# Performance work log

Measured on AMD Instinct MI355X. Metric: run time of the kernel, lower is better.

## Reference

```python
import jax, jax.numpy as jnp
import numpy as np

PAD_token, SOS_token, EOS_token = 0, 1, 2
V, E, H, B, To, Ti = 10000, 512, 512, 32, 256, 1024


def _u(key, shape, fan_in):
    s = 1.0 / np.sqrt(fan_in)
    return jax.random.uniform(key, shape, jnp.float32, -s, s)


def setup_inputs() -> dict:
    key = jax.random.key(0)
    ks = jax.random.split(key, 16)
    inp = {
        "padded_input": jax.random.randint(ks[0], (B, To), 3, V),
        "encoder_padded_outputs": jax.random.normal(ks[1], (B, Ti, H), jnp.float32),
        "embedding": jax.random.normal(ks[2], (V, E), jnp.float32) * 0.02,
        # layer 0 LSTMCell: input = embed + encoder context (E + H)
        "Wih0": _u(ks[3], (4 * H, E + H), H), "Whh0": _u(ks[4], (4 * H, H), H),
        "bih0": _u(ks[5], (4 * H,), H),       "bhh0": _u(ks[6], (4 * H,), H),
        # layer 1 LSTMCell: input = H
        "Wih1": _u(ks[7], (4 * H, H), H),     "Whh1": _u(ks[8], (4 * H, H), H),
        "bih1": _u(ks[9], (4 * H,), H),       "bhh1": _u(ks[10], (4 * H,), H),
        # MLP: Linear(2H -> H), Tanh, Linear(H -> V)
        "W1": _u(ks[11], (H, 2 * H), 2 * H),  "b1": _u(ks[12], (H,), 2 * H),
        "W2": _u(ks[13], (V, H), H),          "b2": _u(ks[14], (V,), H),
    }
    return inp


def _lstm_cell(x, h, c, Wih, Whh, bih, bhh):
    g = x @ Wih.T + bih + h @ Whh.T + bhh            # [B, 4H]
    i, f, gg, o = jnp.split(g, 4, axis=-1)           # torch gate order i,f,g,o
    c2 = jax.nn.sigmoid(f) * c + jax.nn.sigmoid(i) * jnp.tanh(gg)
    h2 = jax.nn.sigmoid(o) * jnp.tanh(c2)
    return h2, c2


def reference(padded_input, encoder_padded_outputs, embedding,
              Wih0, Whh0, bih0, bhh0, Wih1, Whh1, bih1, bhh1,
              W1, b1, W2, b2):
    n = padded_input.shape[0]
    sos = jnp.full((n, 1), SOS_token, padded_input.dtype)
    eos = jnp.full((n, 1), EOS_token, padded_input.dtype)
    ys_in = jnp.concatenate([sos, padded_input], axis=1)   # [B, To+1]
    ys_out = jnp.concatenate([padded_input, eos], axis=1)  # [B, To+1]

    emb = embedding[ys_in]                                 # [B, To+1, E]
    emb_t = jnp.swapaxes(emb, 0, 1)                        # [To+1, B, E]
    enc = encoder_padded_outputs                           # [B, Ti, H]

    h0 = jnp.zeros((n, H), enc.dtype)
    init = (h0, h0, h0, h0, jnp.zeros((n, enc.shape[2]), enc.dtype))

    def step(carry, e_t):
        h_0, c_0, h_1, c_1, att_c = carry
        rnn_in = jnp.concatenate([e_t, att_c], axis=1)
        h_0, c_0 = _lstm_cell(rnn_in, h_0, c_0, Wih0, Whh0, bih0, bhh0)
        h_1, c_1 = _lstm_cell(h_0, h_1, c_1, Wih1, Whh1, bih1, bhh1)
        scores = jnp.einsum('bh,bth->bt', h_1, enc)        # [B, Ti]
        att_w = jax.nn.softmax(scores, axis=-1)
        att_c = jnp.einsum('bt,bth->bh', att_w, enc)       # [B, H]
        mlp_in = jnp.concatenate([h_1, att_c], axis=1)
        logits = jnp.tanh(mlp_in @ W1.T + b1) @ W2.T + b2  # [B, V]
        return (h_0, c_0, h_1, c_1, att_c), logits

    _, y_all = jax.lax.scan(step, init, emb_t)             # [To+1, B, V]
    logits = jnp.swapaxes(y_all, 0, 1).reshape(-1, V)      # [B*(To+1), V]
    labels = ys_out.reshape(-1)
    logp = jax.nn.log_softmax(logits, axis=-1)
    nll = -jnp.take_along_axis(logp, labels[:, None], axis=1)[:, 0]
    mask = (labels != PAD_token).astype(logits.dtype)
    loss = jnp.sum(nll * mask) / jnp.maximum(jnp.sum(mask), 1.0)
    return loss
```

## Files before the change

### kernel.cpp

```cpp
#include <hip/hip_runtime.h>
#include <hip/hip_bf16.h>

#define B_    32
#define TO_   256
#define T_    257
#define H_    512
#define V_    10000
#define TI_   1024
#define NROW_ 8224
#define NB_   256

using f32x4 = __attribute__((ext_vector_type(4))) float;
using s16x8 = __attribute__((ext_vector_type(8))) short;

struct Ptrs {
  const int* padded;
  const float* enc;
  const float* emb;
  const float *Wih0, *Whh0, *bih0, *bhh0;
  const float *Wih1, *Whh1, *bih1, *bhh1;
  const float *W1, *b1, *W2, *b2;
  float* out;
  unsigned short *mlpin;
  unsigned short *embt;
  unsigned short *tanhv;
  unsigned short *W0c;
  unsigned short *W1c;
  unsigned short *W1b;
  unsigned short *W2b;
  float *bias0c, *bias1c;
  float *u;
  unsigned short *Xh0;
  unsigned short *Xh1;
  float *Xh1f;
  float *Zb;
  unsigned *bar;
  float *rowsum;
  float *lablog;
};

__device__ __forceinline__ unsigned short f2b(float f){
  __hip_bfloat16 h = __float2bfloat16(f);
  unsigned short r; __builtin_memcpy(&r, &h, 2); return r;
}
__device__ __forceinline__ float b2f(unsigned short u){
  unsigned v = ((unsigned)u) << 16; float f; __builtin_memcpy(&f, &v, 4); return f;
}
__device__ __forceinline__ float sigf(float x){ return 1.f / (1.f + expf(-x)); }

__device__ __forceinline__ float aldf(const float* p){
  return __hip_atomic_load(p, __ATOMIC_RELAXED, __HIP_MEMORY_SCOPE_AGENT);
}
__device__ __forceinline__ unsigned aldw(const unsigned* p){
  return __hip_atomic_load(p, __ATOMIC_RELAXED, __HIP_MEMORY_SCOPE_AGENT);
}
__device__ __forceinline__ unsigned long long aldu(const unsigned long long* p){
  return __hip_atomic_load(p, __ATOMIC_RELAXED, __HIP_MEMORY_SCOPE_AGENT);
}
__device__ __forceinline__ void astf(float* p, float v){
  __hip_atomic_store(p, v, __ATOMIC_RELAXED, __HIP_MEMORY_SCOPE_AGENT);
}
__device__ __forceinline__ void astu(unsigned long long* p, unsigned long long v){
  __hip_atomic_store(p, v, __ATOMIC_RELAXED, __HIP_MEMORY_SCOPE_AGENT);
}
__device__ __forceinline__ void astw(unsigned* p, unsigned v){
  __hip_atomic_store(p, v, __ATOMIC_RELAXED, __HIP_MEMORY_SCOPE_AGENT);
}

__device__ __forceinline__ void gbar(unsigned* bar, unsigned ph){
  asm volatile("s_waitcnt vmcnt(0)" ::: "memory");
  __syncthreads();
  if (threadIdx.x < 64){
    const int l = threadIdx.x;
    if (l == 0) astw(bar + blockIdx.x * 4, ph);
    for (;;){
      unsigned f0 = aldw(bar + (l      ) * 4);
      unsigned f1 = aldw(bar + (l +  64) * 4);
      unsigned f2 = aldw(bar + (l + 128) * 4);
      unsigned f3 = aldw(bar + (l + 192) * 4);
      bool ok = (f0 >= ph) & (f1 >= ph) & (f2 >= ph) & (f3 >= ph);
      if (__all(ok)) break;
      __builtin_amdgcn_s_sleep(2);
    }
  }
  __syncthreads();
}

__device__ __forceinline__ void gbar128(unsigned* bar, unsigned ph){
  asm volatile("s_waitcnt vmcnt(0)" ::: "memory");
  __syncthreads();
  if (threadIdx.x < 64){
    const int l = threadIdx.x;
    if (l == 0) astw(bar + blockIdx.x * 4, ph);
    for (;;){
      unsigned f0 = aldw(bar + (l     ) * 4);
      unsigned f1 = aldw(bar + (l + 64) * 4);
      bool ok = (f0 >= ph) & (f1 >= ph);
      if (__all(ok)) break;
      __builtin_amdgcn_s_sleep(2);
    }
  }
  __syncthreads();
}

__global__ __launch_bounds__(256) void kprep(Ptrs P){
  const int stride = gridDim.x * blockDim.x;
  const int i0 = blockIdx.x * blockDim.x + threadIdx.x;
  for (int i = i0; i < 2048; i += stride) P.bar[i] = 0u;
  for (int i = i0; i < T_ * B_ * 512; i += stride){
    int k = i & 511, tb = i >> 9, b = tb & 31, t = tb >> 5;
    int tok = (t == 0) ? 1 : P.padded[b * TO_ + (t - 1)];
    P.embt[i] = f2b(P.emb[(size_t)tok * 512 + k]);
  }
  for (int i = i0; i < 2048 * 1536; i += stride){
    int k = i % 1536, gp = i / 1536;
    int j = gp >> 2, q = gp & 3, g = q * 512 + j;
    float v = (k < 1024) ? P.Wih0[(size_t)g * 1024 + k] : P.Whh0[(size_t)g * 512 + (k - 1024)];
    P.W0c[i] = f2b(v);
  }
  for (int i = i0; i < 2048 * 1024; i += stride){
    int k = i & 1023, gp = i >> 10;
    int j = gp >> 2, q = gp & 3, g = q * 512 + j;
    float v = (k < 512) ? P.Wih1[(size_t)g * 512 + k] : P.Whh1[(size_t)g * 512 + (k - 512)];
    P.W1c[i] = f2b(v);
  }
  for (int i = i0; i < 2048; i += stride){
    int j = i >> 2, q = i & 3, g = q * 512 + j;
    P.bias0c[i] = P.bih0[g] + P.bhh0[g];
    P.bias1c[i] = P.bih1[g] + P.bhh1[g];
  }
  for (int i = i0; i < 512 * 1024; i += stride) P.W1b[i] = f2b(P.W1[i]);
  for (int i = i0; i < NROW_; i += stride) P.rowsum[i] = 0.f;
}

__global__ __launch_bounds__(256) void kprep2(Ptrs P){
  const int stride = gridDim.x * blockDim.x;
  const int i0 = blockIdx.x * blockDim.x + threadIdx.x;
  for (int i = i0; i < V_ * 512; i += stride) P.W2b[i] = f2b(P.W2[i]);
}

__global__ __launch_bounds__(256, 1) void kA(Ptrs P){
  __shared__ __align__(16) unsigned short enc_s[128 * 512];
  __shared__ float h1_s[512];
  __shared__ float w_s[128];
  __shared__ float gate_s[32][17];
  __shared__ float h_s[32][4];
  const int bb = blockIdx.x, tid = threadIdx.x;
  const int b_att = bb >> 3;

  {
    const float* ep = P.enc + ((size_t)b_att * TI_ + (size_t)(bb & 7) * 128) * H_;
    for (int idx = tid; idx < 128 * 512; idx += 256){
      int r = idx >> 9;
      unsigned byteoff = ((unsigned)idx * 2u) ^ ((unsigned)(r & 7) << 4);
      enc_s[byteoff >> 1] = f2b(ep[idx]);
    }
  }
  {
    int g = bb * 256 + tid;
    if (g < 32768){ astf(P.u + g, 0.f); astf(P.Xh1f + g, 0.f); }
    if (g < 16384){ astw((unsigned*)P.Xh0 + g, 0u); astw((unsigned*)P.Xh1 + g, 0u); }
    if (g < 64) astf(P.Zb + g, (g >= 32) ? 1.f : 0.f);
  }
  gbar(P.bar, 1u);

  const int wv = tid >> 6;
  const int l  = tid & 63, lr = l & 15, lk = l >> 4;
  const int eidx = tid - 128;
  const int eb = eidx >> 2, ejl = eidx & 3;
  float c0r = 0.f, c1r = 0.f;

  for (int t = 0; t < T_; ++t){
    const int p = t & 1, pp = p ^ 1;
    const unsigned phb = 3u * (unsigned)t;
    if (bb < 128){
      if (wv < 2){
        const int batch = wv * 16 + lr;
        const unsigned short* Brow = P.W0c + (size_t)(bb * 16 + lr) * 1536;
        const unsigned short* Erow = P.embt + ((size_t)t * 32 + batch) * 512;
        const float* Urow = P.u + pp * 16384 + batch * 512;
        const unsigned long long* Hrow =
            (const unsigned long long*)(P.Xh0 + pp * 16384 + batch * 512);
        const float rZ = 1.f / aldf(P.Zb + pp * 32 + batch);
        f32x4 acc = {0.f, 0.f, 0.f, 0.f};
        #pragma unroll
        for (int ks = 0; ks < 16; ++ks){
          s16x8 a = *(const s16x8*)(Erow + ks * 32 + lk * 8);
          s16x8 b = *(const s16x8*)(Brow + ks * 32 + lk * 8);
          acc = __builtin_amdgcn_mfma_f32_16x16x32_bf16(a, b, acc, 0, 0, 0);
        }
        #pragma unroll
        for (int ks = 0; ks < 16; ++ks){
          const int kb = ks * 32 + lk * 8;
          unsigned long long dd[4];
          dd[0] = aldu((const unsigned long long*)(Urow + kb));
          dd[1] = aldu((const unsigned long long*)(Urow + kb + 2));
          dd[2] = aldu((const unsigned long long*)(Urow + kb + 4));
          dd[3] = aldu((const unsigned long long*)(Urow + kb + 6));
          float uf[8]; __builtin_memcpy(uf, dd, 32);
          s16x8 a;
          #pragma unroll
          for (int e = 0; e < 8; ++e) a[e] = (short)f2b(uf[e] * rZ);
          s16x8 b = *(const s16x8*)(Brow + 512 + kb);
          acc = __builtin_amdgcn_mfma_f32_16x16x32_bf16(a, b, acc, 0, 0, 0);
        }
        #pragma unroll
        for (int ks = 0; ks < 16; ++ks){
          const int kb = ks * 32 + lk * 8;
          unsigned long long dd[2];
          dd[0] = aldu(Hrow + (kb >> 2));
          dd[1] = aldu(Hrow + (kb >> 2) + 1);
          s16x8 a; __builtin_memcpy(&a, dd, 16);
          s16x8 b = *(const s16x8*)(Brow + 1024 + kb);
          acc = __builtin_amdgcn_mfma_f32_16x16x32_bf16(a, b, acc, 0, 0, 0);
        }
        #pragma unroll
        for (int j = 0; j < 4; ++j) gate_s[wv * 16 + lk * 4 + j][lr] = acc[j];
      }
    } else if (bb < 160){
      if (t > 0){
        const int b = bb - 128;
        const float rZ = 1.f / aldf(P.Zb + pp * 32 + b);
        unsigned long long v = aldu((const unsigned long long*)(P.u + pp * 16384 + b * 512) + tid);
        float f2[2]; __builtin_memcpy(f2, &v, 8);
        unsigned pk = (unsigned)f2b(f2[0] * rZ) | ((unsigned)f2b(f2[1] * rZ) << 16);
        *(unsigned*)(P.mlpin + ((size_t)(t - 1) * 32 + b) * 1024 + 512 + tid * 2) = pk;
      }
    } else if (bb < 224){
      astf(P.u + p * 16384 + (bb - 160) * 256 + tid, 0.f);
    } else if (bb == 224 && tid < 32){
      astf(P.Zb + p * 32 + tid, 0.f);
    }
    if (bb < 128){
      __syncthreads();
      if (tid >= 128){
        const float* bs = P.bias0c + bb * 16 + ejl * 4;
        float ii = sigf (gate_s[eb][ejl * 4 + 0] + bs[0]);
        float ff = sigf (gate_s[eb][ejl * 4 + 1] + bs[1]);
        float gg = tanhf(gate_s[eb][ejl * 4 + 2] + bs[2]);
        float oo = sigf (gate_s[eb][ejl * 4 + 3] + bs[3]);
        float cn = ff * c0r + ii * gg; c0r = cn;
        h_s[eb][ejl] = oo * tanhf(cn);
      }
      __syncthreads();
      if (tid < 32){
        unsigned short hb[4];
        #pragma unroll
        for (int jl = 0; jl < 4; ++jl) hb[jl] = f2b(h_s[tid][jl]);
        unsigned long long v; __builtin_memcpy(&v, hb, 8);
        astu((unsigned long long*)(P.Xh0 + p * 16384 + tid * 512 + bb * 4), v);
      }
      gbar128(P.bar, phb + 2u);
    }
    if (bb < 128){
      if (wv < 2){
        const int batch = wv * 16 + lr;
        const unsigned short* Brow = P.W1c + (size_t)(bb * 16 + lr) * 1024;
        const unsigned long long* H0r =
            (const unsigned long long*)(P.Xh0 + p * 16384 + batch * 512);
        const unsigned long long* H1r =
            (const unsigned long long*)(P.Xh1 + pp * 16384 + batch * 512);
        f32x4 acc = {0.f, 0.f, 0.f, 0.f};
        #pragma unroll
        for (int ks = 0; ks < 16; ++ks){
          const int kb = ks * 32 + lk * 8;
          unsigned long long dd[2];
          dd[0] = aldu(H0r + (kb >> 2));
          dd[1] = aldu(H0r + (kb >> 2) + 1);
          s16x8 a; __builtin_memcpy(&a, dd, 16);
          s16x8 b = *(const s16x8*)(Brow + kb);
          acc = __builtin_amdgcn_mfma_f32_16x16x32_bf16(a, b, acc, 0, 0, 0);
        }
        #pragma unroll
        for (int ks = 0; ks < 16; ++ks){
          const int kb = ks * 32 + lk * 8;
          unsigned long long dd[2];
          dd[0] = aldu(H1r + (kb >> 2));
          dd[1] = aldu(H1r + (kb >> 2) + 1);
          s16x8 a; __builtin_memcpy(&a, dd, 16);
          s16x8 b = *(const s16x8*)(Brow + 512 + kb);
          acc = __builtin_amdgcn_mfma_f32_16x16x32_bf16(a, b, acc, 0, 0, 0);
        }
        #pragma unroll
        for (int j = 0; j < 4; ++j) gate_s[wv * 16 + lk * 4 + j][lr] = acc[j];
      }
      __syncthreads();
      if (tid >= 128){
        const float* bs = P.bias1c + bb * 16 + ejl * 4;
        float ii = sigf (gate_s[eb][ejl * 4 + 0] + bs[0]);
        float ff = sigf (gate_s[eb][ejl * 4 + 1] + bs[1]);
        float gg = tanhf(gate_s[eb][ejl * 4 + 2] + bs[2]);
        float oo = sigf (gate_s[eb][ejl * 4 + 3] + bs[3]);
        float cn = ff * c1r + ii * gg; c1r = cn;
        h_s[eb][ejl] = oo * tanhf(cn);
      }
      __syncthreads();
      if (tid < 32){
        unsigned short hb[4];
        #pragma unroll
        for (int jl = 0; jl < 4; ++jl) hb[jl] = f2b(h_s[tid][jl]);
        unsigned long long vb; __builtin_memcpy(&vb, hb, 8);
        astu((unsigned long long*)(P.Xh1 + p * 16384 + tid * 512 + bb * 4), vb);
        *(unsigned long long*)(P.mlpin + ((size_t)t * 32 + tid) * 1024 + bb * 4) = vb;
        unsigned long long w0, w1;
        __builtin_memcpy(&w0, &h_s[tid][0], 8);
        __builtin_memcpy(&w1, &h_s[tid][2], 8);
        unsigned long long* dst = (unsigned long long*)P.Xh1f + ((p * 16384 + tid * 512 + bb * 4) >> 1);
        astu(dst, w0); astu(dst + 1, w1);
      }
    }
    gbar(P.bar, phb + 3u);
    {
      unsigned long long v = aldu((const unsigned long long*)(P.Xh1f + p * 16384 + b_att * 512) + tid);
      float f2[2]; __builtin_memcpy(f2, &v, 8);
      h1_s[tid * 2] = f2[0]; h1_s[tid * 2 + 1] = f2[1];
    }
    __syncthreads();
    {
      const int ti_l = tid >> 1, half = tid & 1;
      float s = 0.f;
      const unsigned swz = (unsigned)(ti_l & 7) << 4;
      for (int h8 = half * 256; h8 < half * 256 + 256; h8 += 8){
        unsigned byteoff = ((unsigned)(ti_l * 512 + h8) * 2u) ^ swz;
        s16x8 ev = *(const s16x8*)((const char*)enc_s + byteoff);
        #pragma unroll
        for (int e = 0; e < 8; ++e) s += b2f((unsigned short)ev[e]) * h1_s[h8 + e];
      }
      s += __shfl_xor(s, 1);
      if (half == 0) w_s[ti_l] = expf(s);
    }
    __syncthreads();
    {
      if (tid < 128){
        float z = w_s[tid];
        #pragma unroll
        for (int off = 1; off < 64; off <<= 1) z += __shfl_xor(z, off);
        if ((tid & 63) == 0) unsafeAtomicAdd(P.Zb + p * 32 + b_att, z);
      }
      float a0 = 0.f, a1 = 0.f;
      const int hc = tid * 2;
      for (int ti = 0; ti < 128; ++ti){
        const float wvv = w_s[ti];
        unsigned byteoff = ((unsigned)(ti * 1024 + hc * 2)) ^ ((unsigned)(ti & 7) << 4);
        unsigned pk = *(const unsigned*)((const char*)enc_s + byteoff);
        a0 += wvv * b2f((unsigned short)(pk & 0xffffu));
        a1 += wvv * b2f((unsigned short)(pk >> 16));
      }
      unsafeAtomicAdd(P.u + p * 16384 + b_att * 512 + hc, a0);
      unsafeAtomicAdd(P.u + p * 16384 + b_att * 512 + hc + 1, a1);
    }
    gbar(P.bar, phb + 4u);
  }
  if (bb >= 128 && bb < 160){
    const int b = bb - 128;
    const float rZ = 1.f / aldf(P.Zb + 0 * 32 + b);
    unsigned long long v = aldu((const unsigned long long*)(P.u + 0 * 16384 + b * 512) + tid);
    float f2[2]; __builtin_memcpy(f2, &v, 8);
    unsigned pk = (unsigned)f2b(f2[0] * rZ) | ((unsigned)f2b(f2[1] * rZ) << 16);
    *(unsigned*)(P.mlpin + ((size_t)256 * 32 + b) * 1024 + 512 + tid * 2) = pk;
  }
}

__global__ __launch_bounds__(256) void kB1(Ptrs P){
  const int wid = blockIdx.x * 4 + (threadIdx.x >> 6);
  if (wid >= 129 * 8) return;
  const int mt = wid >> 3, nt = wid & 7;
  const int l = threadIdx.x & 63, lr = l & 15, lk = l >> 4;
  const int mr = mt * 64, nc = nt * 64;
  f32x4 acc[4][4] = {};
  for (int k0 = 0; k0 < 1024; k0 += 32){
    s16x8 af[4], bfm[4];
    #pragma unroll
    for (int f = 0; f < 4; ++f){
      int row = mr + f * 16 + lr; if (row > NROW_ - 1) row = NROW_ - 1;
      af[f] = *(const s16x8*)(P.mlpin + (size_t)row * 1024 + k0 + lk * 8);
      int col = nc + f * 16 + lr;
      bfm[f] = *(const s16x8*)(P.W1b + (size_t)col * 1024 + k0 + lk * 8);
    }
    #pragma unroll
    for (int fi = 0; fi < 4; ++fi)
      #pragma unroll
      for (int fj = 0; fj < 4; ++fj)
        acc[fi][fj] = __builtin_amdgcn_mfma_f32_16x16x32_bf16(af[fi], bfm[fj], acc[fi][fj], 0, 0, 0);
  }
  #pragma unroll
  for (int fi = 0; fi < 4; ++fi){
    #pragma unroll
    for (int jj = 0; jj < 4; ++jj){
      int m = mr + fi * 16 + lk * 4 + jj;
      if (m >= NROW_) continue;
      #pragma unroll
      for (int fj = 0; fj < 4; ++fj){
        int n = nc + fj * 16 + lr;
        P.tanhv[(size_t)m * 512 + n] = f2b(tanhf(acc[fi][fj][jj] + P.b1[n]));
      }
    }
  }
}

__global__ __launch_bounds__(256) void kB2(Ptrs P){
  const int wid = blockIdx.x * 4 + (threadIdx.x >> 6);
  if (wid >= 129 * 157) return;
  const int mt = wid / 157, nt = wid % 157;
  const int l = threadIdx.x & 63, lr = l & 15, lk = l >> 4;
  const int mr = mt * 64, nc = nt * 64;
  f32x4 acc[4][4] = {};
  for (int k0 = 0; k0 < 512; k0 += 32){
    s16x8 af[4], bfm[4];
    #pragma unroll
    for (int f = 0; f < 4; ++f){
      int row = mr + f * 16 + lr; if (row > NROW_ - 1) row = NROW_ - 1;
      af[f] = *(const s16x8*)(P.tanhv + (size_t)row * 512 + k0 + lk * 8);
      int col = nc + f * 16 + lr; if (col > V_ - 1) col = V_ - 1;
      bfm[f] = *(const s16x8*)(P.W2b + (size_t)col * 512 + k0 + lk * 8);
    }
    #pragma unroll
    for (int fi = 0; fi < 4; ++fi)
      #pragma unroll
      for (int fj = 0; fj < 4; ++fj)
        acc[fi][fj] = __builtin_amdgcn_mfma_f32_16x16x32_bf16(af[fi], bfm[fj], acc[fi][fj], 0, 0, 0);
  }
  #pragma unroll
  for (int fi = 0; fi < 4; ++fi){
    #pragma unroll
    for (int jj = 0; jj < 4; ++jj){
      const int m = mr + fi * 16 + lk * 4 + jj;
      float s = 0.f;
      #pragma unroll
      for (int fj = 0; fj < 4; ++fj){
        int n = nc + fj * 16 + lr;
        if (n < V_) s += expf(acc[fi][fj][jj] + P.b2[n]);
      }
      s += __shfl_xor(s, 1); s += __shfl_xor(s, 2);
      s += __shfl_xor(s, 4); s += __shfl_xor(s, 8);
      if (lr == 0 && m < NROW_) unsafeAtomicAdd(P.rowsum + m, s);
    }
  }
}

__global__ __launch_bounds__(256) void kL1(Ptrs P){
  const int wid = blockIdx.x * 4 + (threadIdx.x >> 6);
  if (wid >= NROW_) return;
  const int l = threadIdx.x & 63;
  const int t = wid >> 5, b = wid & 31;
  const int lab = (t < TO_) ? P.padded[b * TO_ + t] : 2;
  float s = 0.f;
  s16x8 av = *(const s16x8*)(P.tanhv + (size_t)wid * 512 + l * 8);
  s16x8 wv = *(const s16x8*)(P.W2b + (size_t)lab * 512 + l * 8);
  #pragma unroll
  for (int e = 0; e < 8; ++e) s += b2f((unsigned short)av[e]) * b2f((unsigned short)wv[e]);
  #pragma unroll
  for (int off = 1; off < 64; off <<= 1) s += __shfl_xor(s, off);
  if (l == 0) P.lablog[wid] = s + P.b2[lab];
}

__global__ __launch_bounds__(512) void kL2(Ptrs P){
  __shared__ float ssum[8], scnt[8];
  const int tid = threadIdx.x;
  float sum = 0.f, cnt = 0.f;
  for (int r = tid; r < NROW_; r += 512){
    int t = r >> 5, b = r & 31;
    int lab = (t < TO_) ? P.padded[b * TO_ + t] : 2;
    if (lab != 0){ sum += logf(P.rowsum[r]) - P.lablog[r]; cnt += 1.f; }
  }
  #pragma unroll
  for (int off = 1; off < 64; off <<= 1){ sum += __shfl_xor(sum, off); cnt += __shfl_xor(cnt, off); }
  if ((tid & 63) == 0){ ssum[tid >> 6] = sum; scnt[tid >> 6] = cnt; }
  __syncthreads();
  if (tid == 0){
    float S = 0.f, C = 0.f;
    for (int i = 0; i < 8; ++i){ S += ssum[i]; C += scnt[i]; }
    P.out[0] = S / fmaxf(C, 1.f);
  }
}

extern "C" void kernel_launch(void* const* d_in, const int* in_sizes, int n_in,
                              void* d_out, int out_size, void* d_ws, size_t ws_size,
                              hipStream_t stream){
  (void)in_sizes; (void)n_in; (void)out_size; (void)ws_size;
  Ptrs P;
  P.padded = (const int*)d_in[0];
  P.enc    = (const float*)d_in[1];
  P.emb    = (const float*)d_in[2];
  P.Wih0 = (const float*)d_in[3];  P.Whh0 = (const float*)d_in[4];
  P.bih0 = (const float*)d_in[5];  P.bhh0 = (const float*)d_in[6];
  P.Wih1 = (const float*)d_in[7];  P.Whh1 = (const float*)d_in[8];
  P.bih1 = (const float*)d_in[9];  P.bhh1 = (const float*)d_in[10];
  P.W1 = (const float*)d_in[11];   P.b1 = (const float*)d_in[12];
  P.W2 = (const float*)d_in[13];   P.b2 = (const float*)d_in[14];
  P.out = (float*)d_out;

  char* w = (char*)d_ws;
  size_t off = 0;
  auto take = [&](size_t bytes) -> void* {
    void* ptr = (void*)(w + off);
    off += (bytes + 255) & ~(size_t)255;
    return ptr;
  };
  P.mlpin  = (unsigned short*)take((size_t)T_ * B_ * 1024 * 2);
  P.embt   = (unsigned short*)take((size_t)T_ * B_ * 512 * 2);
  P.tanhv  = P.embt;
  P.W0c    = (unsigned short*)take((size_t)2048 * 1536 * 2);
  P.W1c    = (unsigned short*)take((size_t)2048 * 1024 * 2);
  P.W2b    = P.W0c;
  P.W1b    = (unsigned short*)take((size_t)512 * 1024 * 2);
  P.bias0c = (float*)take(2048 * 4);
  P.bias1c = (float*)take(2048 * 4);
  P.u      = (float*)take(2 * 32 * 512 * 4);
  P.Xh0    = (unsigned short*)take(2 * 32 * 512 * 2);
  P.Xh1    = (unsigned short*)take(2 * 32 * 512 * 2);
  P.Xh1f   = (float*)take(2 * 32 * 512 * 4);
  P.Zb     = (float*)take(2 * 32 * 4);
  P.bar    = (unsigned*)take(8192);
  P.rowsum = (float*)take(NROW_ * 4);
  P.lablog = (float*)take(NROW_ * 4);

  kprep<<<dim3(2048), dim3(256), 0, stream>>>(P);
  void* args[] = { (void*)&P };
  hipLaunchCooperativeKernel(kA, dim3(NB_), dim3(256), args, 0, stream);
  kprep2<<<dim3(1024), dim3(256), 0, stream>>>(P);
  kB1<<<dim3(258),  dim3(256), 0, stream>>>(P);
  kB2<<<dim3(5064), dim3(256), 0, stream>>>(P);
  kL1<<<dim3(2056), dim3(256), 0, stream>>>(P);
  kL2<<<dim3(1),    dim3(512), 0, stream>>>(P);
}
```

Baseline: 9.451 ms.

## Replace global barriers with targeted flag sync and deterministic attention reduction

Replaces the three full-grid barriers per timestep in the persistent recurrent kernel with point-to-point arrival flags. Layer-0 GEMM blocks wait only on the 32 reducer blocks, the two LSTM layers sync among the 128 GEMM blocks, and attention blocks wait on layer-1 completion. Attention partial sums and softmax denominators are written to per-chunk slots and summed by 32 reducer blocks, replacing global float atomics and the zeroing passes they required. The LSTM GEMMs are also split across all four waves along K, with results combined in shared memory. This aims to cut barrier latency on the sequential critical path, at the cost of more complex dependency reasoning and a risk of ordering bugs.

```diff
diff --git a/kernel.cpp b/kernel.cpp
--- a/kernel.cpp
+++ b/kernel.cpp
@@ -12,6 +12,7 @@
 
 using f32x4 = __attribute__((ext_vector_type(4))) float;
 using s16x8 = __attribute__((ext_vector_type(8))) short;
+typedef unsigned long long ull;
 
 struct Ptrs {
   const int* padded;
@@ -29,12 +30,17 @@
   unsigned short *W1b;
   unsigned short *W2b;
   float *bias0c, *bias1c;
-  float *u;
+  unsigned short *attc;
+  float *upart;
+  float *zp;
   unsigned short *Xh0;
   unsigned short *Xh1;
   float *Xh1f;
-  float *Zb;
-  unsigned *bar;
+  unsigned *arrX;
+  unsigned *arrY;
+  unsigned *marr;
+  unsigned *larr;
+  unsigned *ibar;
   float *rowsum;
   float *lablog;
 };
@@ -54,50 +60,32 @@
 __device__ __forceinline__ unsigned aldw(const unsigned* p){
   return __hip_atomic_load(p, __ATOMIC_RELAXED, __HIP_MEMORY_SCOPE_AGENT);
 }
-__device__ __forceinline__ unsigned long long aldu(const unsigned long long* p){
+__device__ __forceinline__ ull aldu(const ull* p){
   return __hip_atomic_load(p, __ATOMIC_RELAXED, __HIP_MEMORY_SCOPE_AGENT);
 }
 __device__ __forceinline__ void astf(float* p, float v){
   __hip_atomic_store(p, v, __ATOMIC_RELAXED, __HIP_MEMORY_SCOPE_AGENT);
 }
-__device__ __forceinline__ void astu(unsigned long long* p, unsigned long long v){
+__device__ __forceinline__ void astu(ull* p, ull v){
   __hip_atomic_store(p, v, __ATOMIC_RELAXED, __HIP_MEMORY_SCOPE_AGENT);
 }
 __device__ __forceinline__ void astw(unsigned* p, unsigned v){
   __hip_atomic_store(p, v, __ATOMIC_RELAXED, __HIP_MEMORY_SCOPE_AGENT);
 }
-
-__device__ __forceinline__ void gbar(unsigned* bar, unsigned ph){
-  asm volatile("s_waitcnt vmcnt(0)" ::: "memory");
-  __syncthreads();
+#define DRAIN asm volatile("s_waitcnt vmcnt(0)" ::: "memory")
+
+__device__ __forceinline__ void gbarInit(unsigned* bar){
+  DRAIN; __syncthreads();
   if (threadIdx.x < 64){
     const int l = threadIdx.x;
-    if (l == 0) astw(bar + blockIdx.x * 4, ph);
+    if (l == 0) astw(bar + blockIdx.x * 4, 1u);
     for (;;){
       unsigned f0 = aldw(bar + (l      ) * 4);
       unsigned f1 = aldw(bar + (l +  64) * 4);
       unsigned f2 = aldw(bar + (l + 128) * 4);
       unsigned f3 = aldw(bar + (l + 192) * 4);
-      bool ok = (f0 >= ph) & (f1 >= ph) & (f2 >= ph) & (f3 >= ph);
-      if (__all(ok)) break;
-      __builtin_amdgcn_s_sleep(2);
-    }
-  }
-  __syncthreads();
-}
-
-__device__ __forceinline__ void gbar128(unsigned* bar, unsigned ph){
-  asm volatile("s_waitcnt vmcnt(0)" ::: "memory");
-  __syncthreads();
-  if (threadIdx.x < 64){
-    const int l = threadIdx.x;
-    if (l == 0) astw(bar + blockIdx.x * 4, ph);
-    for (;;){
-      unsigned f0 = aldw(bar + (l     ) * 4);
-      unsigned f1 = aldw(bar + (l + 64) * 4);
-      bool ok = (f0 >= ph) & (f1 >= ph);
-      if (__all(ok)) break;
-      __builtin_amdgcn_s_sleep(2);
+      if (__all((f0 >= 1u) & (f1 >= 1u) & (f2 >= 1u) & (f3 >= 1u))) break;
+      __builtin_amdgcn_s_sleep(1);
     }
   }
   __syncthreads();
@@ -106,7 +94,9 @@
 __global__ __launch_bounds__(256) void kprep(Ptrs P){
   const int stride = gridDim.x * blockDim.x;
   const int i0 = blockIdx.x * blockDim.x + threadIdx.x;
-  for (int i = i0; i < 2048; i += stride) P.bar[i] = 0u;
+  for (int i = i0; i < 128 * 4; i += stride){ P.arrX[i] = 0u; P.arrY[i] = 0u; }
+  for (int i = i0; i < 256 * 4; i += stride){ P.marr[i] = 0u; P.ibar[i] = 0u; }
+  for (int i = i0; i < 32 * 4; i += stride) P.larr[i] = 0u;
   for (int i = i0; i < T_ * B_ * 512; i += stride){
     int k = i & 511, tb = i >> 9, b = tb & 31, t = tb >> 5;
     int tok = (t == 0) ? 1 : P.padded[b * TO_ + (t - 1)];
@@ -143,13 +133,14 @@
   __shared__ __align__(16) unsigned short enc_s[128 * 512];
   __shared__ float h1_s[512];
   __shared__ float w_s[128];
-  __shared__ float gate_s[32][17];
+  __shared__ float gate_s[2][32][17];
   __shared__ float h_s[32][4];
+  __shared__ float zred[2];
   const int bb = blockIdx.x, tid = threadIdx.x;
-  const int b_att = bb >> 3;
+  const int b_att = bb >> 3, tc = bb & 7;
 
   {
-    const float* ep = P.enc + ((size_t)b_att * TI_ + (size_t)(bb & 7) * 128) * H_;
+    const float* ep = P.enc + ((size_t)b_att * TI_ + (size_t)tc * 128) * H_;
     for (int idx = tid; idx < 128 * 512; idx += 256){
       int r = idx >> 9;
       unsigned byteoff = ((unsigned)idx * 2u) ^ ((unsigned)(r & 7) << 4);
@@ -158,87 +149,72 @@
   }
   {
     int g = bb * 256 + tid;
-    if (g < 32768){ astf(P.u + g, 0.f); astf(P.Xh1f + g, 0.f); }
     if (g < 16384){ astw((unsigned*)P.Xh0 + g, 0u); astw((unsigned*)P.Xh1 + g, 0u); }
-    if (g < 64) astf(P.Zb + g, (g >= 32) ? 1.f : 0.f);
-  }
-  gbar(P.bar, 1u);
-
-  const int wv = tid >> 6;
-  const int l  = tid & 63, lr = l & 15, lk = l >> 4;
-  const int eidx = tid - 128;
-  const int eb = eidx >> 2, ejl = eidx & 3;
+    if (g < 32768) astf(P.Xh1f + g, 0.f);
+    if (g < 8192)  astw((unsigned*)P.attc + g, 0u);
+  }
+  gbarInit(P.ibar);
+
+  const int wv = tid >> 6, l = tid & 63, lr = l & 15, lk = l >> 4;
+  const int bh = wv & 1, kh = wv >> 1;
+  const int batch = bh * 16 + lr;
+  const int eidx = tid - 128, eb = eidx >> 2, ejl = eidx & 3;
+  const bool isGemm = bb < 128;
+  const int rb = bb - 128; const bool isRed = (rb >= 0 && rb < 32);
   float c0r = 0.f, c1r = 0.f;
 
   for (int t = 0; t < T_; ++t){
     const int p = t & 1, pp = p ^ 1;
-    const unsigned phb = 3u * (unsigned)t;
-    if (bb < 128){
-      if (wv < 2){
-        const int batch = wv * 16 + lr;
+    const unsigned tv = (unsigned)t + 1u;
+    if (isGemm){
+      if (t > 0 && tid < 64){
+        const unsigned want = tv - 1u;
+        for (;;){
+          unsigned f = (tid < 32) ? aldw(P.larr + tid * 4) : want;
+          if (__all(f >= want)) break;
+          __builtin_amdgcn_s_sleep(1);
+        }
+      }
+      __syncthreads();
+      {
         const unsigned short* Brow = P.W0c + (size_t)(bb * 16 + lr) * 1536;
         const unsigned short* Erow = P.embt + ((size_t)t * 32 + batch) * 512;
-        const float* Urow = P.u + pp * 16384 + batch * 512;
-        const unsigned long long* Hrow =
-            (const unsigned long long*)(P.Xh0 + pp * 16384 + batch * 512);
-        const float rZ = 1.f / aldf(P.Zb + pp * 32 + batch);
+        const ull* Arow = (const ull*)(P.attc + batch * 512);
+        const ull* Hrow = (const ull*)(P.Xh0 + pp * 16384 + batch * 512);
         f32x4 acc = {0.f, 0.f, 0.f, 0.f};
         #pragma unroll
-        for (int ks = 0; ks < 16; ++ks){
-          s16x8 a = *(const s16x8*)(Erow + ks * 32 + lk * 8);
-          s16x8 b = *(const s16x8*)(Brow + ks * 32 + lk * 8);
+        for (int ks = 0; ks < 8; ++ks){
+          const int kb = (kh * 8 + ks) * 32 + lk * 8;
+          s16x8 a = *(const s16x8*)(Erow + kb);
+          s16x8 b = *(const s16x8*)(Brow + kb);
           acc = __builtin_amdgcn_mfma_f32_16x16x32_bf16(a, b, acc, 0, 0, 0);
         }
         #pragma unroll
-        for (int ks = 0; ks < 16; ++ks){
-          const int kb = ks * 32 + lk * 8;
-          unsigned long long dd[4];
-          dd[0] = aldu((const unsigned long long*)(Urow + kb));
-          dd[1] = aldu((const unsigned long long*)(Urow + kb + 2));
-          dd[2] = aldu((const unsigned long long*)(Urow + kb + 4));
-          dd[3] = aldu((const unsigned long long*)(Urow + kb + 6));
-          float uf[8]; __builtin_memcpy(uf, dd, 32);
-          s16x8 a;
-          #pragma unroll
-          for (int e = 0; e < 8; ++e) a[e] = (short)f2b(uf[e] * rZ);
+        for (int ks = 0; ks < 8; ++ks){
+          const int kb = (kh * 8 + ks) * 32 + lk * 8;
+          ull d0 = aldu(Arow + (kb >> 2)), d1 = aldu(Arow + (kb >> 2) + 1);
+          s16x8 a; __builtin_memcpy(&a, &d0, 8); __builtin_memcpy(((char*)&a) + 8, &d1, 8);
           s16x8 b = *(const s16x8*)(Brow + 512 + kb);
           acc = __builtin_amdgcn_mfma_f32_16x16x32_bf16(a, b, acc, 0, 0, 0);
         }
         #pragma unroll
-        for (int ks = 0; ks < 16; ++ks){
-          const int kb = ks * 32 + lk * 8;
-          unsigned long long dd[2];
-          dd[0] = aldu(Hrow + (kb >> 2));
-          dd[1] = aldu(Hrow + (kb >> 2) + 1);
-          s16x8 a; __builtin_memcpy(&a, dd, 16);
+        for (int ks = 0; ks < 8; ++ks){
+          const int kb = (kh * 8 + ks) * 32 + lk * 8;
+          ull d0 = aldu(Hrow + (kb >> 2)), d1 = aldu(Hrow + (kb >> 2) + 1);
+          s16x8 a; __builtin_memcpy(&a, &d0, 8); __builtin_memcpy(((char*)&a) + 8, &d1, 8);
           s16x8 b = *(const s16x8*)(Brow + 1024 + kb);
           acc = __builtin_amdgcn_mfma_f32_16x16x32_bf16(a, b, acc, 0, 0, 0);
         }
         #pragma unroll
-        for (int j = 0; j < 4; ++j) gate_s[wv * 16 + lk * 4 + j][lr] = acc[j];
-      }
-    } else if (bb < 160){
-      if (t > 0){
-        const int b = bb - 128;
-        const float rZ = 1.f / aldf(P.Zb + pp * 32 + b);
-        unsigned long long v = aldu((const unsigned long long*)(P.u + pp * 16384 + b * 512) + tid);
-        float f2[2]; __builtin_memcpy(f2, &v, 8);
-        unsigned pk = (unsigned)f2b(f2[0] * rZ) | ((unsigned)f2b(f2[1] * rZ) << 16);
-        *(unsigned*)(P.mlpin + ((size_t)(t - 1) * 32 + b) * 1024 + 512 + tid * 2) = pk;
-      }
-    } else if (bb < 224){
-      astf(P.u + p * 16384 + (bb - 160) * 256 + tid, 0.f);
-    } else if (bb == 224 && tid < 32){
-      astf(P.Zb + p * 32 + tid, 0.f);
-    }
-    if (bb < 128){
+        for (int j = 0; j < 4; ++j) gate_s[kh][bh * 16 + lk * 4 + j][lr] = acc[j];
+      }
       __syncthreads();
       if (tid >= 128){
         const float* bs = P.bias0c + bb * 16 + ejl * 4;
-        float ii = sigf (gate_s[eb][ejl * 4 + 0] + bs[0]);
-        float ff = sigf (gate_s[eb][ejl * 4 + 1] + bs[1]);
-        float gg = tanhf(gate_s[eb][ejl * 4 + 2] + bs[2]);
-        float oo = sigf (gate_s[eb][ejl * 4 + 3] + bs[3]);
+        float ii = sigf (gate_s[0][eb][ejl * 4 + 0] + gate_s[1][eb][ejl * 4 + 0] + bs[0]);
+        float ff = sigf (gate_s[0][eb][ejl * 4 + 1] + gate_s[1][eb][ejl * 4 + 1] + bs[1]);
+        float gg = tanhf(gate_s[0][eb][ejl * 4 + 2] + gate_s[1][eb][ejl * 4 + 2] + bs[2]);
+        float oo = sigf (gate_s[0][eb][ejl * 4 + 3] + gate_s[1][eb][ejl * 4 + 3] + bs[3]);
         float cn = ff * c0r + ii * gg; c0r = cn;
         h_s[eb][ejl] = oo * tanhf(cn);
       }
@@ -247,50 +223,50 @@
         unsigned short hb[4];
         #pragma unroll
         for (int jl = 0; jl < 4; ++jl) hb[jl] = f2b(h_s[tid][jl]);
-        unsigned long long v; __builtin_memcpy(&v, hb, 8);
-        astu((unsigned long long*)(P.Xh0 + p * 16384 + tid * 512 + bb * 4), v);
-      }
-      gbar128(P.bar, phb + 2u);
-    }
-    if (bb < 128){
-      if (wv < 2){
-        const int batch = wv * 16 + lr;
+        ull v; __builtin_memcpy(&v, hb, 8);
+        astu((ull*)(P.Xh0 + p * 16384 + tid * 512 + bb * 4), v);
+      }
+      DRAIN; __syncthreads();
+      if (tid < 64){
+        if (tid == 0) astw(P.arrX + bb * 4, tv);
+        for (;;){
+          unsigned f0 = aldw(P.arrX + tid * 4), f1 = aldw(P.arrX + (tid + 64) * 4);
+          if (__all((f0 >= tv) & (f1 >= tv))) break;
+          __builtin_amdgcn_s_sleep(1);
+        }
+      }
+      __syncthreads();
+      {
         const unsigned short* Brow = P.W1c + (size_t)(bb * 16 + lr) * 1024;
-        const unsigned long long* H0r =
-            (const unsigned long long*)(P.Xh0 + p * 16384 + batch * 512);
-        const unsigned long long* H1r =
-            (const unsigned long long*)(P.Xh1 + pp * 16384 + batch * 512);
+        const ull* H0r = (const ull*)(P.Xh0 + p * 16384 + batch * 512);
+        const ull* H1r = (const ull*)(P.Xh1 + pp * 16384 + batch * 512);
         f32x4 acc = {0.f, 0.f, 0.f, 0.f};
         #pragma unroll
-        for (int ks = 0; ks < 16; ++ks){
-          const int kb = ks * 32 + lk * 8;
-          unsigned long long dd[2];
-          dd[0] = aldu(H0r + (kb >> 2));
-          dd[1] = aldu(H0r + (kb >> 2) + 1);
-          s16x8 a; __builtin_memcpy(&a, dd, 16);
+        for (int ks = 0; ks < 8; ++ks){
+          const int kb = (kh * 8 + ks) * 32 + lk * 8;
+          ull d0 = aldu(H0r + (kb >> 2)), d1 = aldu(H0r + (kb >> 2) + 1);
+          s16x8 a; __builtin_memcpy(&a, &d0, 8); __builtin_memcpy(((char*)&a) + 8, &d1, 8);
           s16x8 b = *(const s16x8*)(Brow + kb);
           acc = __builtin_amdgcn_mfma_f32_16x16x32_bf16(a, b, acc, 0, 0, 0);
         }
         #pragma unroll
-        for (int ks = 0; ks < 16; ++ks){
-          const int kb = ks * 32 + lk * 8;
-          unsigned long long dd[2];
-          dd[0] = aldu(H1r + (kb >> 2));
-          dd[1] = aldu(H1r + (kb >> 2) + 1);
-          s16x8 a; __builtin_memcpy(&a, dd, 16);
+        for (int ks = 0; ks < 8; ++ks){
+          const int kb = (kh * 8 + ks) * 32 + lk * 8;
+          ull d0 = aldu(H1r + (kb >> 2)), d1 = aldu(H1r + (kb >> 2) + 1);
+          s16x8 a; __builtin_memcpy(&a, &d0, 8); __builtin_memcpy(((char*)&a) + 8, &d1, 8);
           s16x8 b = *(const s16x8*)(Brow + 512 + kb);
           acc = __builtin_amdgcn_mfma_f32_16x16x32_bf16(a, b, acc, 0, 0, 0);
         }
         #pragma unroll
-        for (int j = 0; j < 4; ++j) gate_s[wv * 16 + lk * 4 + j][lr] = acc[j];
+        for (int j = 0; j < 4; ++j) gate_s[kh][bh * 16 + lk * 4 + j][lr] = acc[j];
       }
       __syncthreads();
       if (tid >= 128){
         const float* bs = P.bias1c + bb * 16 + ejl * 4;
-        float ii = sigf (gate_s[eb][ejl * 4 + 0] + bs[0]);
-        float ff = sigf (gate_s[eb][ejl * 4 + 1] + bs[1]);
-        float gg = tanhf(gate_s[eb][ejl * 4 + 2] + bs[2]);
-        float oo = sigf (gate_s[eb][ejl * 4 + 3] + bs[3]);
+        float ii = sigf (gate_s[0][eb][ejl * 4 + 0] + gate_s[1][eb][ejl * 4 + 0] + bs[0]);
+        float ff = sigf (gate_s[0][eb][ejl * 4 + 1] + gate_s[1][eb][ejl * 4 + 1] + bs[1]);
+        float gg = tanhf(gate_s[0][eb][ejl * 4 + 2] + gate_s[1][eb][ejl * 4 + 2] + bs[2]);
+        float oo = sigf (gate_s[0][eb][ejl * 4 + 3] + gate_s[1][eb][ejl * 4 + 3] + bs[3]);
         float cn = ff * c1r + ii * gg; c1r = cn;
         h_s[eb][ejl] = oo * tanhf(cn);
       }
@@ -299,19 +275,28 @@
         unsigned short hb[4];
         #pragma unroll
         for (int jl = 0; jl < 4; ++jl) hb[jl] = f2b(h_s[tid][jl]);
-        unsigned long long vb; __builtin_memcpy(&vb, hb, 8);
-        astu((unsigned long long*)(P.Xh1 + p * 16384 + tid * 512 + bb * 4), vb);
-        *(unsigned long long*)(P.mlpin + ((size_t)t * 32 + tid) * 1024 + bb * 4) = vb;
-        unsigned long long w0, w1;
+        ull vb; __builtin_memcpy(&vb, hb, 8);
+        astu((ull*)(P.Xh1 + p * 16384 + tid * 512 + bb * 4), vb);
+        *(ull*)(P.mlpin + ((size_t)t * 32 + tid) * 1024 + bb * 4) = vb;
+        ull w0, w1;
         __builtin_memcpy(&w0, &h_s[tid][0], 8);
         __builtin_memcpy(&w1, &h_s[tid][2], 8);
-        unsigned long long* dst = (unsigned long long*)P.Xh1f + ((p * 16384 + tid * 512 + bb * 4) >> 1);
+        ull* dst = (ull*)P.Xh1f + ((p * 16384 + tid * 512 + bb * 4) >> 1);
         astu(dst, w0); astu(dst + 1, w1);
       }
-    }
-    gbar(P.bar, phb + 3u);
+      DRAIN; __syncthreads();
+      if (tid == 0) astw(P.arrY + bb * 4, tv);
+    }
+    if (tid < 64){
+      for (;;){
+        unsigned f0 = aldw(P.arrY + tid * 4), f1 = aldw(P.arrY + (tid + 64) * 4);
+        if (__all((f0 >= tv) & (f1 >= tv))) break;
+        __builtin_amdgcn_s_sleep(1);
+      }
+    }
+    __syncthreads();
     {
-      unsigned long long v = aldu((const unsigned long long*)(P.Xh1f + p * 16384 + b_att * 512) + tid);
+      ull v = aldu((const ull*)(P.Xh1f + p * 16384 + b_att * 512) + tid);
       float f2[2]; __builtin_memcpy(f2, &v, 8);
       h1_s[tid * 2] = f2[0]; h1_s[tid * 2 + 1] = f2[1];
     }
@@ -335,7 +320,7 @@
         float z = w_s[tid];
         #pragma unroll
         for (int off = 1; off < 64; off <<= 1) z += __shfl_xor(z, off);
-        if ((tid & 63) == 0) unsafeAtomicAdd(P.Zb + p * 32 + b_att, z);
+        if ((tid & 63) == 0) zred[tid >> 6] = z;
       }
       float a0 = 0.f, a1 = 0.f;
       const int hc = tid * 2;
@@ -346,18 +331,39 @@
         a0 += wvv * b2f((unsigned short)(pk & 0xffffu));
         a1 += wvv * b2f((unsigned short)(pk >> 16));
       }
-      unsafeAtomicAdd(P.u + p * 16384 + b_att * 512 + hc, a0);
-      unsafeAtomicAdd(P.u + p * 16384 + b_att * 512 + hc + 1, a1);
-    }
-    gbar(P.bar, phb + 4u);
-  }
-  if (bb >= 128 && bb < 160){
-    const int b = bb - 128;
-    const float rZ = 1.f / aldf(P.Zb + 0 * 32 + b);
-    unsigned long long v = aldu((const unsigned long long*)(P.u + 0 * 16384 + b * 512) + tid);
-    float f2[2]; __builtin_memcpy(f2, &v, 8);
-    unsigned pk = (unsigned)f2b(f2[0] * rZ) | ((unsigned)f2b(f2[1] * rZ) << 16);
-    *(unsigned*)(P.mlpin + ((size_t)256 * 32 + b) * 1024 + 512 + tid * 2) = pk;
+      float f2[2] = {a0, a1};
+      ull pv; __builtin_memcpy(&pv, f2, 8);
+      astu((ull*)(P.upart + ((size_t)b_att * 8 + tc) * 512 + hc), pv);
+      __syncthreads();
+      if (tid == 0) astf(P.zp + b_att * 8 + tc, zred[0] + zred[1]);
+      DRAIN; __syncthreads();
+      if (tid == 0) astw(P.marr + (b_att * 8 + tc) * 4, tv);
+    }
+    if (isRed){
+      if (tid < 64){
+        for (;;){
+          unsigned f = (tid < 8) ? aldw(P.marr + (rb * 8 + tid) * 4) : tv;
+          if (__all(f >= tv)) break;
+          __builtin_amdgcn_s_sleep(1);
+        }
+      }
+      __syncthreads();
+      const int hc = tid * 2;
+      float s0 = 0.f, s1 = 0.f, zs = 0.f;
+      #pragma unroll
+      for (int c = 0; c < 8; ++c){
+        ull v = aldu((const ull*)(P.upart + ((size_t)rb * 8 + c) * 512 + hc));
+        float f2[2]; __builtin_memcpy(f2, &v, 8);
+        s0 += f2[0]; s1 += f2[1];
+        zs += aldf(P.zp + rb * 8 + c);
+      }
+      const float rZ = 1.f / zs;
+      unsigned pk = (unsigned)f2b(s0 * rZ) | ((unsigned)f2b(s1 * rZ) << 16);
+      astw(((unsigned*)P.attc) + rb * 256 + tid, pk);
+      *(unsigned*)(P.mlpin + ((size_t)t * 32 + rb) * 1024 + 512 + hc) = pk;
+      DRAIN; __syncthreads();
+      if (tid == 0) astw(P.larr + rb * 4, tv);
+    }
   }
 }
 
@@ -506,12 +512,17 @@
   P.W1b    = (unsigned short*)take((size_t)512 * 1024 * 2);
   P.bias0c = (float*)take(2048 * 4);
   P.bias1c = (float*)take(2048 * 4);
-  P.u      = (float*)take(2 * 32 * 512 * 4);
+  P.attc   = (unsigned short*)take(32 * 512 * 2);
+  P.upart  = (float*)take((size_t)32 * 8 * 512 * 4);
+  P.zp     = (float*)take(32 * 8 * 4);
   P.Xh0    = (unsigned short*)take(2 * 32 * 512 * 2);
   P.Xh1    = (unsigned short*)take(2 * 32 * 512 * 2);
   P.Xh1f   = (float*)take(2 * 32 * 512 * 4);
-  P.Zb     = (float*)take(2 * 32 * 4);
-  P.bar    = (unsigned*)take(8192);
+  P.arrX   = (unsigned*)take(128 * 4 * 4);
+  P.arrY   = (unsigned*)take(128 * 4 * 4);
+  P.marr   = (unsigned*)take(256 * 4 * 4);
+  P.larr   = (unsigned*)take(32 * 4 * 4);
+  P.ibar   = (unsigned*)take(256 * 4 * 4);
   P.rowsum = (float*)take(NROW_ * 4);
   P.lablog = (float*)take(NROW_ * 4);
 
```

Result: faster. 7.714 ms (-18.4%).
